# Performance work log

Measured on AMD Instinct MI355X. Metric: run time of the kernel, lower is better.

The kernel has to match this reference:

```python
import jax, jax.numpy as jnp
import numpy as np

H = 32      # num attention heads
HD = 64     # head dim
RD = 16     # rotary dim = 0.25 * head_dim (partial rotary)
EPS = 1e-5
BASE = 10000.0


def _ln(x, w, b):
    m = x.mean(-1, keepdims=True)
    v = ((x - m) ** 2).mean(-1, keepdims=True)
    return (x - m) / jnp.sqrt(v + EPS) * w + b


def _rot_half(x):
    x1, x2 = jnp.split(x, 2, axis=-1)
    return jnp.concatenate([-x2, x1], axis=-1)


def setup_inputs() -> dict:
    key = jax.random.key(0)
    ks = jax.random.split(key, 16)
    B, S, D, FF = 1, 2048, 2048, 8192
    std = 0.02
    hidden_states = jax.random.normal(ks[0], (B, S, D), jnp.float32)
    memory = jax.random.normal(ks[1], (B, S, D), jnp.float32)
    # causal additive mask (B,1,S,S): 0 where allowed, -inf above diagonal
    causal = jnp.where(jnp.tril(jnp.ones((S, S), bool)), 0.0, -jnp.inf).astype(jnp.float32)
    attention_mask = jnp.broadcast_to(causal[None, None], (B, 1, S, S))
    position_ids = jnp.broadcast_to(jnp.arange(S, dtype=jnp.int32), (B, S))
    return {
        'hidden_states': hidden_states,
        'memory': memory,
        'attention_mask': attention_mask,
        'position_ids': position_ids,
        'ln1_w': jnp.ones((D,), jnp.float32),
        'ln1_b': jnp.zeros((D,), jnp.float32),
        'ln2_w': jnp.ones((D,), jnp.float32),
        'ln2_b': jnp.zeros((D,), jnp.float32),
        'Wq': jax.random.normal(ks[2], (D, D), jnp.float32) * std,
        'Wk': jax.random.normal(ks[3], (D, D), jnp.float32) * std,
        'Wv': jax.random.normal(ks[4], (D, D), jnp.float32) * std,
        'Wo': jax.random.normal(ks[5], (D, D), jnp.float32) * std,
        'Wg': jax.random.normal(ks[6], (FF, D), jnp.float32) * std,
        'Wu': jax.random.normal(ks[7], (FF, D), jnp.float32) * std,
        'Wd': jax.random.normal(ks[8], (D, FF), jnp.float32) * std,
    }


def reference(hidden_states, memory, attention_mask, position_ids,
              ln1_w, ln1_b, ln2_w, ln2_b, Wq, Wk, Wv, Wo, Wg, Wu, Wd):
    B, S, D = hidden_states.shape
    residual = hidden_states
    h = _ln(hidden_states, ln1_w, ln1_b)
    mem = _ln(memory, ln1_w, ln1_b)

    # fast_forward: concat memory in front along sequence
    x = jnp.concatenate([mem, h], axis=1)              # (B, 2S, D)
    pos = jnp.concatenate([position_ids, position_ids], axis=1)  # (B, 2S)
    L = 2 * S

    q = (x @ Wq.T).reshape(B, L, H, HD).transpose(0, 2, 1, 3)  # (B,H,2S,HD)
    k = (x @ Wk.T).reshape(B, L, H, HD).transpose(0, 2, 1, 3)
    v = (x @ Wv.T).reshape(B, L, H, HD).transpose(0, 2, 1, 3)

    # partial rotary embedding
    inv_freq = 1.0 / (BASE ** (jnp.arange(0, RD, 2, dtype=jnp.float32) / RD))
    t = pos.astype(jnp.float32)[:, :, None] * inv_freq       # (B,2S,RD/2)
    emb = jnp.concatenate([t, t], axis=-1)                   # (B,2S,RD)
    cos = jnp.cos(emb)[:, None]                              # (B,1,2S,RD)
    sin = jnp.sin(emb)[:, None]
    qr, qp = q[..., :RD], q[..., RD:]
    kr, kp = k[..., :RD], k[..., RD:]
    qr = qr * cos + _rot_half(qr) * sin
    kr = kr * cos + _rot_half(kr) * sin
    q = jnp.concatenate([qr, qp], axis=-1)
    k = jnp.concatenate([kr, kp], axis=-1)

    # only non-memory queries attend
    q = q[:, :, S:]                                          # (B,H,S,HD)
    scores = jnp.einsum('bhqd,bhkd->bhqk', q, k) / jnp.sqrt(jnp.float32(HD))  # (B,H,S,2S)

    # left mask: causal + no attending to own memory slot; right: only own position (+ causal)
    eye = jnp.eye(S, dtype=bool)[None, None]
    left = jnp.where(eye, -jnp.inf, attention_mask)
    right = jnp.where(eye, attention_mask, -jnp.inf)
    mask = jnp.concatenate([left, right], axis=-1)           # (B,1,S,2S)

    w = jax.nn.softmax((scores + mask).astype(jnp.float32), axis=-1).astype(q.dtype)
    attn = jnp.einsum('bhqk,bhkd->bhqd', w, v)
    attn = attn.transpose(0, 2, 1, 3).reshape(B, S, D) @ Wo.T

    h = residual + attn
    residual2 = h
    h2 = _ln(h, ln2_w, ln2_b)
    mlp = (jax.nn.silu(h2 @ Wg.T) * (h2 @ Wu.T)) @ Wd.T
    return residual2 + mlp
```

## Files before the change

kernel.cpp:

```cpp
#include <hip/hip_runtime.h>
#include <stdint.h>
#include <stddef.h>

typedef short s16;
typedef __attribute__((ext_vector_type(8))) short short8;
typedef __attribute__((ext_vector_type(4))) float float4v;

#define S_LEN 2048
#define DMODEL 2048
#define LLEN 4096
#define FFDIM 8192
#define NHEAD 32
#define HDIM 64

#define AS1 __attribute__((address_space(1)))
#define AS3 __attribute__((address_space(3)))

__device__ __forceinline__ float bf2f(short s) {
  union { uint32_t u; float f; } x;
  x.u = ((uint32_t)(uint16_t)s) << 16;
  return x.f;
}
__device__ __forceinline__ short f2bf(float f) {
  union { float f; uint32_t u; } x;
  x.f = f;
  uint32_t r = x.u + 0x7fffu + ((x.u >> 16) & 1u);
  return (short)(r >> 16);
}

template <typename T> __device__ __forceinline__ float ldv(const T* p, size_t i);
template <> __device__ __forceinline__ float ldv<float>(const float* p, size_t i) { return p[i]; }
template <> __device__ __forceinline__ float ldv<s16>(const s16* p, size_t i) { return bf2f(p[i]); }
template <typename T> __device__ __forceinline__ void stv(T* p, size_t i, float v);
template <> __device__ __forceinline__ void stv<float>(float* p, size_t i, float v) { p[i] = v; }
template <> __device__ __forceinline__ void stv<s16>(s16* p, size_t i, float v) { p[i] = f2bf(v); }

__global__ __launch_bounds__(256) void w2bf(const float* __restrict__ src, s16* __restrict__ dst,
                                            int n8) {
  const int i = blockIdx.x * 256 + threadIdx.x;
  if (i >= n8) return;
  const float4v a = ((const float4v*)src)[2 * i];
  const float4v b = ((const float4v*)src)[2 * i + 1];
  short8 o;
#pragma unroll
  for (int j = 0; j < 4; j++) { o[j] = f2bf(a[j]); o[j + 4] = f2bf(b[j]); }
  ((short8*)dst)[i] = o;
}

template <typename T>
__global__ __launch_bounds__(256) void ln_kernel(const T* __restrict__ src,
                                                 const float* __restrict__ w,
                                                 const float* __restrict__ b,
                                                 s16* __restrict__ dst) {
  const int row = blockIdx.x, t = threadIdx.x;
  float v[8];
  float s = 0.f, s2 = 0.f;
#pragma unroll
  for (int i = 0; i < 8; i++) {
    v[i] = ldv<T>(src, (size_t)row * DMODEL + t * 8 + i);
    s += v[i];
    s2 += v[i] * v[i];
  }
#pragma unroll
  for (int off = 32; off > 0; off >>= 1) {
    s += __shfl_down(s, off);
    s2 += __shfl_down(s2, off);
  }
  __shared__ float rs[4], rs2[4];
  if ((t & 63) == 0) { rs[t >> 6] = s; rs2[t >> 6] = s2; }
  __syncthreads();
  const float fs = rs[0] + rs[1] + rs[2] + rs[3];
  const float fs2 = rs2[0] + rs2[1] + rs2[2] + rs2[3];
  const float mean = fs * (1.f / (float)DMODEL);
  const float var = fs2 * (1.f / (float)DMODEL) - mean * mean;
  const float rstd = rsqrtf(var + 1e-5f);
  const float4v w0 = *(const float4v*)(w + t * 8);
  const float4v w1 = *(const float4v*)(w + t * 8 + 4);
  const float4v b0 = *(const float4v*)(b + t * 8);
  const float4v b1 = *(const float4v*)(b + t * 8 + 4);
  short8 o;
#pragma unroll
  for (int i = 0; i < 4; i++) {
    o[i] = f2bf((v[i] - mean) * rstd * w0[i] + b0[i]);
    o[i + 4] = f2bf((v[i + 4] - mean) * rstd * w1[i] + b1[i]);
  }
  *(short8*)(dst + (size_t)row * DMODEL + t * 8) = o;
}

__global__ __launch_bounds__(256) void init_out(float4v* __restrict__ dst,
                                                const float4v* __restrict__ src, int n4) {
  const int i = blockIdx.x * 256 + threadIdx.x;
  if (i < n4) dst[i] = src ? src[i] : float4v{0.f, 0.f, 0.f, 0.f};
}

template <typename T>
__global__ __launch_bounds__(256) void rope_kernel(T* __restrict__ buf, const int* __restrict__ pos,
                                                   int nrows) {
  const int idx = blockIdx.x * 256 + threadIdx.x;
  if (idx >= nrows * NHEAD) return;
  const int row = idx >> 5, h = idx & 31;
  const int pid = pos[row < S_LEN ? row : row - S_LEN];
  T* ptr = buf + (size_t)row * DMODEL + h * HDIM;
  float a[8], c[8];
  if constexpr (sizeof(T) == 2) {
    const short8 r0 = *(const short8*)ptr;
    const short8 r1 = *(const short8*)(ptr + 8);
#pragma unroll
    for (int f = 0; f < 8; f++) { a[f] = bf2f(r0[f]); c[f] = bf2f(r1[f]); }
  } else {
    const float4v x0 = *(const float4v*)ptr;
    const float4v x1 = *(const float4v*)(ptr + 4);
    const float4v x2 = *(const float4v*)(ptr + 8);
    const float4v x3 = *(const float4v*)(ptr + 12);
#pragma unroll
    for (int f = 0; f < 4; f++) { a[f] = x0[f]; a[f + 4] = x1[f]; c[f] = x2[f]; c[f + 4] = x3[f]; }
  }
  const float inv_freq[8] = {1.0f, 0.31622776601683794f, 0.1f, 0.031622776601683794f,
                             0.01f, 0.0031622776601683794f, 0.001f, 0.00031622776601683794f};
  const float fp = (float)pid;
  float o0[8], o1[8];
#pragma unroll
  for (int f = 0; f < 8; f++) {
    float sv, cv;
    sincosf(fp * inv_freq[f], &sv, &cv);
    o0[f] = a[f] * cv - c[f] * sv;
    o1[f] = c[f] * cv + a[f] * sv;
  }
  if constexpr (sizeof(T) == 2) {
    short8 w0, w1;
#pragma unroll
    for (int f = 0; f < 8; f++) { w0[f] = f2bf(o0[f]); w1[f] = f2bf(o1[f]); }
    *(short8*)ptr = w0;
    *(short8*)(ptr + 8) = w1;
  } else {
    float4v y0, y1, y2, y3;
#pragma unroll
    for (int f = 0; f < 4; f++) { y0[f] = o0[f]; y1[f] = o0[f + 4]; y2[f] = o1[f]; y3[f] = o1[f + 4]; }
    *(float4v*)ptr = y0;
    *(float4v*)(ptr + 4) = y1;
    *(float4v*)(ptr + 8) = y2;
    *(float4v*)(ptr + 12) = y3;
  }
}

template <int EPI, int BSRC, typename AUXT, typename OUTT>
__global__ __launch_bounds__(256) void gemm_bt(const s16* __restrict__ A, const void* __restrict__ Wp,
                                               OUTT* __restrict__ C, const AUXT* __restrict__ aux,
                                               int M, int N, int K) {
  __shared__ alignas(16) s16 As[3][128 * 32];
  __shared__ alignas(16) s16 Bs[3][128 * 32];
  const int t = threadIdx.x;
  const int wave = t >> 6, lane = t & 63;
  const int quad = lane >> 4, l15 = lane & 15;
  const int n0 = blockIdx.x * 128, m0 = blockIdx.y * 128;
  const int wm = wave >> 1, wn = wave & 1;
  const int srow = lane >> 2, skk = (lane & 3) * 8;
  const int br4 = t >> 2, bc4 = (t & 3) * 8;
  const int kchunk = K / (int)gridDim.z;
  const int kbeg = kchunk * (int)blockIdx.z;

  float4v acc[4][4];
#pragma unroll
  for (int i = 0; i < 4; i++)
#pragma unroll
    for (int j = 0; j < 4; j++) acc[i][j] = float4v{0.f, 0.f, 0.f, 0.f};

  const s16* Wb = (const s16*)Wp;

  if constexpr (BSRC == 1) {
    const int nsteps = kchunk >> 5;
    auto stage = [&](int buf, int k0) {
#pragma unroll
      for (int cc = 0; cc < 2; cc++) {
        const int ci = wave * 2 + cc;
        const s16* ga = A + (size_t)(m0 + ci * 16 + srow) * K + (k0 + skk);
        __builtin_amdgcn_global_load_lds((const AS1 void*)ga, (AS3 void*)(&As[buf][ci * 512]), 16, 0, 0);
        const s16* gb = Wb + (size_t)(n0 + ci * 16 + srow) * K + (k0 + skk);
        __builtin_amdgcn_global_load_lds((const AS1 void*)gb, (AS3 void*)(&Bs[buf][ci * 512]), 16, 0, 0);
      }
    };
    stage(0, kbeg);
    if (nsteps > 1) {
      stage(1, kbeg + 32);
      asm volatile("s_waitcnt vmcnt(4)" ::: "memory");
    } else {
      asm volatile("s_waitcnt vmcnt(0)" ::: "memory");
    }
    __builtin_amdgcn_s_barrier();
    asm volatile("" ::: "memory");
    int cur = 0;
    for (int s = 0; s < nsteps; ++s) {
      short8 a[4], b[4];
#pragma unroll
      for (int mt = 0; mt < 4; mt++)
        a[mt] = *(const short8*)&As[cur][(wm * 64 + mt * 16 + l15) * 32 + quad * 8];
#pragma unroll
      for (int nt = 0; nt < 4; nt++)
        b[nt] = *(const short8*)&Bs[cur][(wn * 64 + nt * 16 + l15) * 32 + quad * 8];
      if (s + 2 < nsteps) {
        int nb = cur + 2; if (nb >= 3) nb -= 3;
        stage(nb, kbeg + (s + 2) * 32);
      }
#pragma unroll
      for (int mt = 0; mt < 4; mt++)
#pragma unroll
        for (int nt = 0; nt < 4; nt++)
          acc[mt][nt] = __builtin_amdgcn_mfma_f32_16x16x32_bf16(a[mt], b[nt], acc[mt][nt], 0, 0, 0);
      if (s + 1 < nsteps) {
        if (s + 2 < nsteps) asm volatile("s_waitcnt vmcnt(4)" ::: "memory");
        else asm volatile("s_waitcnt vmcnt(0)" ::: "memory");
        __builtin_amdgcn_s_barrier();
        asm volatile("" ::: "memory");
      }
      cur = (cur == 2) ? 0 : cur + 1;
    }
  } else {
    const float* wrow0 = (const float*)Wp + (size_t)(n0 + br4) * K + bc4;
    const float* wrow1 = wrow0 + (size_t)64 * K;
    for (int k0 = kbeg; k0 < kbeg + kchunk; k0 += 32) {
      float4v wa0 = *(const float4v*)(wrow0 + k0);
      float4v wa1 = *(const float4v*)(wrow0 + k0 + 4);
      float4v wb0 = *(const float4v*)(wrow1 + k0);
      float4v wb1 = *(const float4v*)(wrow1 + k0 + 4);
      __syncthreads();
#pragma unroll
      for (int cc = 0; cc < 2; cc++) {
        const int ci = wave * 2 + cc;
        const s16* ga = A + (size_t)(m0 + ci * 16 + srow) * K + (k0 + skk);
        __builtin_amdgcn_global_load_lds((const AS1 void*)ga, (AS3 void*)(&As[0][ci * 512]), 16, 0, 0);
      }
      short8 c0, c1;
#pragma unroll
      for (int i = 0; i < 4; i++) {
        c0[i] = f2bf(wa0[i]);
        c0[i + 4] = f2bf(wa1[i]);
        c1[i] = f2bf(wb0[i]);
        c1[i + 4] = f2bf(wb1[i]);
      }
      *(short8*)&Bs[0][br4 * 32 + bc4] = c0;
      *(short8*)&Bs[0][(64 + br4) * 32 + bc4] = c1;
      __syncthreads();
      short8 a[4], b[4];
#pragma unroll
      for (int mt = 0; mt < 4; mt++)
        a[mt] = *(const short8*)&As[0][(wm * 64 + mt * 16 + l15) * 32 + quad * 8];
#pragma unroll
      for (int nt = 0; nt < 4; nt++)
        b[nt] = *(const short8*)&Bs[0][(wn * 64 + nt * 16 + l15) * 32 + quad * 8];
#pragma unroll
      for (int mt = 0; mt < 4; mt++)
#pragma unroll
        for (int nt = 0; nt < 4; nt++)
          acc[mt][nt] = __builtin_amdgcn_mfma_f32_16x16x32_bf16(a[mt], b[nt], acc[mt][nt], 0, 0, 0);
    }
  }
#pragma unroll
  for (int mt = 0; mt < 4; mt++) {
#pragma unroll
    for (int nt = 0; nt < 4; nt++) {
      const float* av = (const float*)&acc[mt][nt];
      const int col = n0 + wn * 64 + nt * 16 + l15;
      const int rowb = m0 + wm * 64 + mt * 16 + quad * 4;
#pragma unroll
      for (int r = 0; r < 4; r++) {
        const size_t idx = (size_t)(rowb + r) * N + col;
        float v = av[r];
        if constexpr (EPI == 3) {
          unsafeAtomicAdd((float*)&C[idx], v);
        } else {
          if (EPI == 1) v += ldv<AUXT>(aux, idx);
          if (EPI == 2) { const float g = ldv<AUXT>(aux, idx); v *= g / (1.0f + __expf(-g)); }
          stv<OUTT>(C, idx, v);
        }
      }
    }
  }
}

__global__ __launch_bounds__(256) void attn_kernel(const float* __restrict__ qb, const s16* __restrict__ kb,
                                                   const s16* __restrict__ vb, s16* __restrict__ attn) {
  __shared__ alignas(16) s16 Qs[64 * 72];
  __shared__ alignas(16) s16 Ks[64 * 72];
  __shared__ alignas(16) s16 Vt[64 * 72];
  __shared__ alignas(16) s16 Ps[64 * 72];
  const int t = threadIdx.x;
  const int h = blockIdx.x & 31;
  const int qblk = 31 - (int)(blockIdx.x >> 5);
  const int wave = t >> 6, lane = t & 63;
  const int quad = lane >> 4, l15 = lane & 15;

#pragma unroll
  for (int rr = 0; rr < 2; rr++) {
    const int tt = t + rr * 256;
    const int i = tt >> 3, d0 = (tt & 7) * 8;
    const float* qp = qb + (size_t)(qblk * 64 + i) * DMODEL + h * HDIM + d0;
    const float4v q0 = *(const float4v*)qp;
    const float4v q1 = *(const float4v*)(qp + 4);
    short8 o;
#pragma unroll
    for (int x = 0; x < 4; x++) { o[x] = f2bf(q0[x]); o[x + 4] = f2bf(q1[x]); }
    *(short8*)&Qs[i * 72 + d0] = o;
  }

  float4v O[4];
#pragma unroll
  for (int i = 0; i < 4; i++) O[i] = float4v{0.f, 0.f, 0.f, 0.f};
  float m_run[4] = {-1e30f, -1e30f, -1e30f, -1e30f};
  float l_run[4] = {0.f, 0.f, 0.f, 0.f};

  const float SCALE = 0.125f * 1.442695040888963f;

  const int j0 = t >> 3, d00 = (t & 7) * 8;
  const int vkeyw = (d00 >> 3) & 7;
  const size_t colb = (size_t)h * HDIM + d00;

  const int nchunks = qblk + 2;
  short8 kr0 = *(const short8*)(kb + (size_t)j0 * DMODEL + colb);
  short8 kr1 = *(const short8*)(kb + (size_t)(j0 + 32) * DMODEL + colb);
  short8 vr0 = *(const short8*)(vb + (size_t)j0 * DMODEL + colb);
  short8 vr1 = *(const short8*)(vb + (size_t)(j0 + 32) * DMODEL + colb);

  for (int c = 0; c < nchunks; ++c) {
    asm volatile("s_waitcnt lgkmcnt(0)" ::: "memory");
    __builtin_amdgcn_s_barrier();
    asm volatile("" ::: "memory");
    *(short8*)&Ks[j0 * 72 + d00] = kr0;
    *(short8*)&Ks[(j0 + 32) * 72 + d00] = kr1;
#pragma unroll
    for (int x = 0; x < 8; x++) {
      Vt[(d00 + x) * 72 + (j0 ^ (vkeyw << 3))] = vr0[x];
      Vt[(d00 + x) * 72 + ((j0 + 32) ^ (vkeyw << 3))] = vr1[x];
    }
    if (c + 1 < nchunks) {
      const int krow = (c + 1 <= qblk) ? (c + 1) * 64 : (S_LEN + qblk * 64);
      kr0 = *(const short8*)(kb + (size_t)(krow + j0) * DMODEL + colb);
      kr1 = *(const short8*)(kb + (size_t)(krow + j0 + 32) * DMODEL + colb);
      vr0 = *(const short8*)(vb + (size_t)(krow + j0) * DMODEL + colb);
      vr1 = *(const short8*)(vb + (size_t)(krow + j0 + 32) * DMODEL + colb);
    }
    asm volatile("s_waitcnt lgkmcnt(0)" ::: "memory");
    __builtin_amdgcn_s_barrier();
    asm volatile("" ::: "memory");

    float4v Sacc[4];
#pragma unroll
    for (int i = 0; i < 4; i++) Sacc[i] = float4v{0.f, 0.f, 0.f, 0.f};
    __builtin_amdgcn_s_setprio(1);
#pragma unroll
    for (int ks = 0; ks < 2; ks++) {
      const short8 af = *(const short8*)&Qs[(wave * 16 + l15) * 72 + ks * 32 + quad * 8];
#pragma unroll
      for (int nt = 0; nt < 4; nt++) {
        const short8 bf = *(const short8*)&Ks[(nt * 16 + l15) * 72 + ks * 32 + quad * 8];
        Sacc[nt] = __builtin_amdgcn_mfma_f32_16x16x32_bf16(af, bf, Sacc[nt], 0, 0, 0);
      }
    }
    __builtin_amdgcn_s_setprio(0);
    float* sp = (float*)Sacc;
    if (c < qblk) {
#pragma unroll
      for (int i = 0; i < 16; i++) sp[i] = fminf(sp[i] * SCALE, 2e4f);
    } else {
#pragma unroll
      for (int nt = 0; nt < 4; nt++)
#pragma unroll
        for (int r = 0; r < 4; r++) {
          const int il = wave * 16 + quad * 4 + r;
          const int jl = nt * 16 + l15;
          const bool ok = (c == qblk) ? (jl < il) : (jl == il);
          sp[nt * 4 + r] = ok ? fminf(sp[nt * 4 + r] * SCALE, 2e4f) : -1e30f;
        }
    }
#pragma unroll
    for (int r = 0; r < 4; r++) {
      float mx = fmaxf(fmaxf(sp[0 * 4 + r], sp[1 * 4 + r]), fmaxf(sp[2 * 4 + r], sp[3 * 4 + r]));
#pragma unroll
      for (int off = 1; off < 16; off <<= 1) mx = fmaxf(mx, __shfl_xor(mx, off));
      const float mnew = fmaxf(m_run[r], mx);
      float alpha, sum;
      if (mnew < -1e29f) {
        alpha = 1.f; sum = 0.f;
#pragma unroll
        for (int nt = 0; nt < 4; nt++) sp[nt * 4 + r] = 0.f;
      } else {
        alpha = exp2f(m_run[r] - mnew);
        m_run[r] = mnew;
        sum = 0.f;
#pragma unroll
        for (int nt = 0; nt < 4; nt++) {
          const float p = exp2f(sp[nt * 4 + r] - mnew);
          sp[nt * 4 + r] = p;
          sum += p;
        }
      }
#pragma unroll
      for (int off = 1; off < 16; off <<= 1) sum += __shfl_xor(sum, off);
      l_run[r] = l_run[r] * alpha + sum;
      float* op = (float*)O;
#pragma unroll
      for (int dt = 0; dt < 4; dt++) op[dt * 4 + r] *= alpha;
    }
#pragma unroll
    for (int nt = 0; nt < 4; nt++)
#pragma unroll
      for (int r = 0; r < 4; r++)
        Ps[(wave * 16 + quad * 4 + r) * 72 + nt * 16 + l15] = f2bf(sp[nt * 4 + r]);
    __builtin_amdgcn_s_setprio(1);
#pragma unroll
    for (int ks = 0; ks < 2; ks++) {
      const short8 pf = *(const short8*)&Ps[(wave * 16 + l15) * 72 + ks * 32 + quad * 8];
#pragma unroll
      for (int dt = 0; dt < 4; dt++) {
        const int dd = dt * 16 + l15;
        const int vkey = (dd >> 3) & 7;
        const short8 vf = *(const short8*)&Vt[dd * 72 + ((ks * 32 + quad * 8) ^ (vkey << 3))];
        O[dt] = __builtin_amdgcn_mfma_f32_16x16x32_bf16(pf, vf, O[dt], 0, 0, 0);
      }
    }
    __builtin_amdgcn_s_setprio(0);
  }
  const float* op = (const float*)O;
#pragma unroll
  for (int dt = 0; dt < 4; dt++)
#pragma unroll
    for (int r = 0; r < 4; r++) {
      const int row = qblk * 64 + wave * 16 + quad * 4 + r;
      const int col = h * HDIM + dt * 16 + l15;
      const float inv_l = 1.0f / fmaxf(l_run[r], 1e-20f);
      attn[(size_t)row * DMODEL + col] = f2bf(op[dt * 4 + r] * inv_l);
    }
}

extern "C" void kernel_launch(void* const* d_in, const int* in_sizes, int n_in,
                              void* d_out, int out_size, void* d_ws, size_t ws_size,
                              hipStream_t stream) {
  const float* hidden = (const float*)d_in[0];
  const float* memory = (const float*)d_in[1];
  const int* pos_ids = (const int*)d_in[3];
  const float* ln1_w = (const float*)d_in[4];
  const float* ln1_b = (const float*)d_in[5];
  const float* ln2_w = (const float*)d_in[6];
  const float* ln2_b = (const float*)d_in[7];
  const float* Wq = (const float*)d_in[8];
  const float* Wk = (const float*)d_in[9];
  const float* Wv = (const float*)d_in[10];
  const float* Wo = (const float*)d_in[11];
  const float* Wg = (const float*)d_in[12];
  const float* Wu = (const float*)d_in[13];
  const float* Wd = (const float*)d_in[14];
  s16* ws = (s16*)d_ws;
  const size_t M1 = (size_t)1024 * 1024;

  s16* x = ws;
  float* q = (float*)d_out;
  s16* k = ws + 8 * M1;
  s16* v = ws + 16 * M1;
  s16* attn = ws;
  s16* h2 = ws + 4 * M1;
  s16* g = ws + 8 * M1;

  const bool bw = ws_size >= (size_t)88 * M1 * sizeof(s16);
  s16* Wqb = ws + 24 * M1;
  s16* Wkb = Wqb + 4 * M1;
  s16* Wvb = Wkb + 4 * M1;
  s16* Wob = Wvb + 4 * M1;
  s16* Wgb = Wob + 4 * M1;
  s16* Wub = Wgb + 16 * M1;
  s16* Wdb = Wub + 16 * M1;

  if (bw) {
    w2bf<<<2048, 256, 0, stream>>>(Wq, Wqb, 512 * 1024);
    w2bf<<<2048, 256, 0, stream>>>(Wk, Wkb, 512 * 1024);
    w2bf<<<2048, 256, 0, stream>>>(Wv, Wvb, 512 * 1024);
    w2bf<<<2048, 256, 0, stream>>>(Wo, Wob, 512 * 1024);
    w2bf<<<8192, 256, 0, stream>>>(Wg, Wgb, 2048 * 1024);
    w2bf<<<8192, 256, 0, stream>>>(Wu, Wub, 2048 * 1024);
    w2bf<<<8192, 256, 0, stream>>>(Wd, Wdb, 2048 * 1024);
  }

  ln_kernel<float><<<S_LEN, 256, 0, stream>>>(memory, ln1_w, ln1_b, x);
  ln_kernel<float><<<S_LEN, 256, 0, stream>>>(hidden, ln1_w, ln1_b, x + (size_t)S_LEN * DMODEL);
  init_out<<<4096, 256, 0, stream>>>((float4v*)d_out, (const float4v*)nullptr, 1 << 20);
  if (bw) {
    gemm_bt<3, 1, float, float><<<dim3(16, 16, 4), 256, 0, stream>>>(x + (size_t)S_LEN * DMODEL, Wqb, q, (const float*)nullptr, S_LEN, DMODEL, DMODEL);
    gemm_bt<0, 1, s16, s16><<<dim3(16, 32), 256, 0, stream>>>(x, Wkb, k, (const s16*)nullptr, LLEN, DMODEL, DMODEL);
    gemm_bt<0, 1, s16, s16><<<dim3(16, 32), 256, 0, stream>>>(x, Wvb, v, (const s16*)nullptr, LLEN, DMODEL, DMODEL);
  } else {
    gemm_bt<3, 0, float, float><<<dim3(16, 16, 4), 256, 0, stream>>>(x + (size_t)S_LEN * DMODEL, Wq, q, (const float*)nullptr, S_LEN, DMODEL, DMODEL);
    gemm_bt<0, 0, s16, s16><<<dim3(16, 32), 256, 0, stream>>>(x, Wk, k, (const s16*)nullptr, LLEN, DMODEL, DMODEL);
    gemm_bt<0, 0, s16, s16><<<dim3(16, 32), 256, 0, stream>>>(x, Wv, v, (const s16*)nullptr, LLEN, DMODEL, DMODEL);
  }
  rope_kernel<float><<<(S_LEN * NHEAD) / 256, 256, 0, stream>>>(q, pos_ids, S_LEN);
  rope_kernel<s16><<<(LLEN * NHEAD) / 256, 256, 0, stream>>>(k, pos_ids, LLEN);
  attn_kernel<<<NHEAD * (S_LEN / 64), 256, 0, stream>>>(q, k, v, attn);
  init_out<<<4096, 256, 0, stream>>>((float4v*)d_out, (const float4v*)hidden, 1 << 20);
  if (bw)
    gemm_bt<3, 1, float, float><<<dim3(16, 16, 4), 256, 0, stream>>>(attn, Wob, (float*)d_out, (const float*)nullptr, S_LEN, DMODEL, DMODEL);
  else
    gemm_bt<3, 0, float, float><<<dim3(16, 16, 4), 256, 0, stream>>>(attn, Wo, (float*)d_out, (const float*)nullptr, S_LEN, DMODEL, DMODEL);
  ln_kernel<float><<<S_LEN, 256, 0, stream>>>((const float*)d_out, ln2_w, ln2_b, h2);
  if (bw) {
    gemm_bt<0, 1, s16, s16><<<dim3(64, 16), 256, 0, stream>>>(h2, Wgb, g, (const s16*)nullptr, S_LEN, FFDIM, DMODEL);
    gemm_bt<2, 1, s16, s16><<<dim3(64, 16), 256, 0, stream>>>(h2, Wub, g, g, S_LEN, FFDIM, DMODEL);
    gemm_bt<3, 1, float, float><<<dim3(16, 16, 4), 256, 0, stream>>>(g, Wdb, (float*)d_out, (const float*)nullptr, S_LEN, DMODEL, FFDIM);
  } else {
    gemm_bt<0, 0, s16, s16><<<dim3(64, 16), 256, 0, stream>>>(h2, Wg, g, (const s16*)nullptr, S_LEN, FFDIM, DMODEL);
    gemm_bt<2, 0, s16, s16><<<dim3(64, 16), 256, 0, stream>>>(h2, Wu, g, g, S_LEN, FFDIM, DMODEL);
    gemm_bt<3, 0, float, float><<<dim3(16, 16, 4), 256, 0, stream>>>(g, Wd, (float*)d_out, (const float*)nullptr, S_LEN, DMODEL, FFDIM);
  }
}
```

Before: 942.5 us.

## Use 256x256 tiled 512-thread GEMM with 4-stage pipeline and fused K/V projection

Adds a bf16-weight GEMM kernel with 256x256 output tiles, 8 waves and a 4-deep LDS prefetch ring, and uses it for all projection GEMMs on the bf16-weight path. K and V projections become one GEMM over contiguous Wk|Wv bf16 weights, writing an interleaved KV buffer with a 2*D leading dimension. Rope and attention now take that stride. The larger tiles raise operand reuse per load but use more LDS and registers and give fewer blocks per GEMM.

```diff
diff --git a/kernel.cpp b/kernel.cpp
--- a/kernel.cpp
+++ b/kernel.cpp
@@ -95,12 +95,12 @@
 
 template <typename T>
 __global__ __launch_bounds__(256) void rope_kernel(T* __restrict__ buf, const int* __restrict__ pos,
-                                                   int nrows) {
+                                                   int nrows, int ld) {
   const int idx = blockIdx.x * 256 + threadIdx.x;
   if (idx >= nrows * NHEAD) return;
   const int row = idx >> 5, h = idx & 31;
   const int pid = pos[row < S_LEN ? row : row - S_LEN];
-  T* ptr = buf + (size_t)row * DMODEL + h * HDIM;
+  T* ptr = buf + (size_t)row * ld + h * HDIM;
   float a[8], c[8];
   if constexpr (sizeof(T) == 2) {
     const short8 r0 = *(const short8*)ptr;
@@ -143,124 +143,78 @@
   }
 }
 
-template <int EPI, int BSRC, typename AUXT, typename OUTT>
-__global__ __launch_bounds__(256) void gemm_bt(const s16* __restrict__ A, const void* __restrict__ Wp,
-                                               OUTT* __restrict__ C, const AUXT* __restrict__ aux,
-                                               int M, int N, int K) {
-  __shared__ alignas(16) s16 As[3][128 * 32];
-  __shared__ alignas(16) s16 Bs[3][128 * 32];
+template <int EPI, typename AUXT, typename OUTT>
+__global__ __launch_bounds__(512, 2) void gemm_bt2(const s16* __restrict__ A, const s16* __restrict__ W,
+                                                   OUTT* __restrict__ C, const AUXT* __restrict__ aux,
+                                                   int M, int N, int K) {
+  __shared__ alignas(16) s16 As[4][256 * 32];
+  __shared__ alignas(16) s16 Bs[4][256 * 32];
   const int t = threadIdx.x;
   const int wave = t >> 6, lane = t & 63;
   const int quad = lane >> 4, l15 = lane & 15;
-  const int n0 = blockIdx.x * 128, m0 = blockIdx.y * 128;
-  const int wm = wave >> 1, wn = wave & 1;
+  const int n0 = blockIdx.x * 256, m0 = blockIdx.y * 256;
+  const int wm = wave >> 2, wn = wave & 3;
   const int srow = lane >> 2, skk = (lane & 3) * 8;
-  const int br4 = t >> 2, bc4 = (t & 3) * 8;
   const int kchunk = K / (int)gridDim.z;
   const int kbeg = kchunk * (int)blockIdx.z;
-
-  float4v acc[4][4];
-#pragma unroll
-  for (int i = 0; i < 4; i++)
+  const int nsteps = kchunk >> 5;
+
+  float4v acc[8][4];
+#pragma unroll
+  for (int i = 0; i < 8; i++)
 #pragma unroll
     for (int j = 0; j < 4; j++) acc[i][j] = float4v{0.f, 0.f, 0.f, 0.f};
 
-  const s16* Wb = (const s16*)Wp;
-
-  if constexpr (BSRC == 1) {
-    const int nsteps = kchunk >> 5;
-    auto stage = [&](int buf, int k0) {
-#pragma unroll
-      for (int cc = 0; cc < 2; cc++) {
-        const int ci = wave * 2 + cc;
-        const s16* ga = A + (size_t)(m0 + ci * 16 + srow) * K + (k0 + skk);
-        __builtin_amdgcn_global_load_lds((const AS1 void*)ga, (AS3 void*)(&As[buf][ci * 512]), 16, 0, 0);
-        const s16* gb = Wb + (size_t)(n0 + ci * 16 + srow) * K + (k0 + skk);
-        __builtin_amdgcn_global_load_lds((const AS1 void*)gb, (AS3 void*)(&Bs[buf][ci * 512]), 16, 0, 0);
-      }
-    };
-    stage(0, kbeg);
-    if (nsteps > 1) {
-      stage(1, kbeg + 32);
-      asm volatile("s_waitcnt vmcnt(4)" ::: "memory");
-    } else {
-      asm volatile("s_waitcnt vmcnt(0)" ::: "memory");
-    }
-    __builtin_amdgcn_s_barrier();
-    asm volatile("" ::: "memory");
-    int cur = 0;
-    for (int s = 0; s < nsteps; ++s) {
-      short8 a[4], b[4];
-#pragma unroll
-      for (int mt = 0; mt < 4; mt++)
-        a[mt] = *(const short8*)&As[cur][(wm * 64 + mt * 16 + l15) * 32 + quad * 8];
+  auto stage = [&](int buf, int k0) {
+#pragma unroll
+    for (int cc = 0; cc < 2; cc++) {
+      const int ci = wave * 2 + cc;
+      const s16* ga = A + (size_t)(m0 + ci * 16 + srow) * K + (k0 + skk);
+      __builtin_amdgcn_global_load_lds((const AS1 void*)ga, (AS3 void*)(&As[buf][ci * 512]), 16, 0, 0);
+      const s16* gb = W + (size_t)(n0 + ci * 16 + srow) * K + (k0 + skk);
+      __builtin_amdgcn_global_load_lds((const AS1 void*)gb, (AS3 void*)(&Bs[buf][ci * 512]), 16, 0, 0);
+    }
+  };
+  stage(0, kbeg);
+  if (nsteps > 1) stage(1, kbeg + 32);
+  if (nsteps > 2) stage(2, kbeg + 64);
+  if (nsteps > 2) asm volatile("s_waitcnt vmcnt(8)" ::: "memory");
+  else if (nsteps > 1) asm volatile("s_waitcnt vmcnt(4)" ::: "memory");
+  else asm volatile("s_waitcnt vmcnt(0)" ::: "memory");
+  __builtin_amdgcn_s_barrier();
+  asm volatile("" ::: "memory");
+
+  int cur = 0;
+  for (int s = 0; s < nsteps; ++s) {
+    short8 a[8], b[4];
+#pragma unroll
+    for (int mt = 0; mt < 8; mt++)
+      a[mt] = *(const short8*)&As[cur][(wm * 128 + mt * 16 + l15) * 32 + quad * 8];
+#pragma unroll
+    for (int nt = 0; nt < 4; nt++)
+      b[nt] = *(const short8*)&Bs[cur][(wn * 64 + nt * 16 + l15) * 32 + quad * 8];
+    if (s + 3 < nsteps) stage((cur + 3) & 3, kbeg + (s + 3) * 32);
+#pragma unroll
+    for (int mt = 0; mt < 8; mt++)
 #pragma unroll
       for (int nt = 0; nt < 4; nt++)
-        b[nt] = *(const short8*)&Bs[cur][(wn * 64 + nt * 16 + l15) * 32 + quad * 8];
-      if (s + 2 < nsteps) {
-        int nb = cur + 2; if (nb >= 3) nb -= 3;
-        stage(nb, kbeg + (s + 2) * 32);
-      }
-#pragma unroll
-      for (int mt = 0; mt < 4; mt++)
-#pragma unroll
-        for (int nt = 0; nt < 4; nt++)
-          acc[mt][nt] = __builtin_amdgcn_mfma_f32_16x16x32_bf16(a[mt], b[nt], acc[mt][nt], 0, 0, 0);
-      if (s + 1 < nsteps) {
-        if (s + 2 < nsteps) asm volatile("s_waitcnt vmcnt(4)" ::: "memory");
-        else asm volatile("s_waitcnt vmcnt(0)" ::: "memory");
-        __builtin_amdgcn_s_barrier();
-        asm volatile("" ::: "memory");
-      }
-      cur = (cur == 2) ? 0 : cur + 1;
-    }
-  } else {
-    const float* wrow0 = (const float*)Wp + (size_t)(n0 + br4) * K + bc4;
-    const float* wrow1 = wrow0 + (size_t)64 * K;
-    for (int k0 = kbeg; k0 < kbeg + kchunk; k0 += 32) {
-      float4v wa0 = *(const float4v*)(wrow0 + k0);
-      float4v wa1 = *(const float4v*)(wrow0 + k0 + 4);
-      float4v wb0 = *(const float4v*)(wrow1 + k0);
-      float4v wb1 = *(const float4v*)(wrow1 + k0 + 4);
-      __syncthreads();
-#pragma unroll
-      for (int cc = 0; cc < 2; cc++) {
-        const int ci = wave * 2 + cc;
-        const s16* ga = A + (size_t)(m0 + ci * 16 + srow) * K + (k0 + skk);
-        __builtin_amdgcn_global_load_lds((const AS1 void*)ga, (AS3 void*)(&As[0][ci * 512]), 16, 0, 0);
-      }
-      short8 c0, c1;
-#pragma unroll
-      for (int i = 0; i < 4; i++) {
-        c0[i] = f2bf(wa0[i]);
-        c0[i + 4] = f2bf(wa1[i]);
-        c1[i] = f2bf(wb0[i]);
-        c1[i + 4] = f2bf(wb1[i]);
-      }
-      *(short8*)&Bs[0][br4 * 32 + bc4] = c0;
-      *(short8*)&Bs[0][(64 + br4) * 32 + bc4] = c1;
-      __syncthreads();
-      short8 a[4], b[4];
-#pragma unroll
-      for (int mt = 0; mt < 4; mt++)
-        a[mt] = *(const short8*)&As[0][(wm * 64 + mt * 16 + l15) * 32 + quad * 8];
-#pragma unroll
-      for (int nt = 0; nt < 4; nt++)
-        b[nt] = *(const short8*)&Bs[0][(wn * 64 + nt * 16 + l15) * 32 + quad * 8];
-#pragma unroll
-      for (int mt = 0; mt < 4; mt++)
-#pragma unroll
-        for (int nt = 0; nt < 4; nt++)
-          acc[mt][nt] = __builtin_amdgcn_mfma_f32_16x16x32_bf16(a[mt], b[nt], acc[mt][nt], 0, 0, 0);
-    }
-  }
-#pragma unroll
-  for (int mt = 0; mt < 4; mt++) {
+        acc[mt][nt] = __builtin_amdgcn_mfma_f32_16x16x32_bf16(a[mt], b[nt], acc[mt][nt], 0, 0, 0);
+    if (s + 1 < nsteps) {
+      if (s + 3 < nsteps) asm volatile("s_waitcnt vmcnt(8)" ::: "memory");
+      else if (s + 2 < nsteps) asm volatile("s_waitcnt vmcnt(4)" ::: "memory");
+      else asm volatile("s_waitcnt vmcnt(0)" ::: "memory");
+      __builtin_amdgcn_s_barrier();
+      asm volatile("" ::: "memory");
+    }
+    cur = (cur + 1) & 3;
+  }
+#pragma unroll
+  for (int mt = 0; mt < 8; mt++) {
 #pragma unroll
     for (int nt = 0; nt < 4; nt++) {
       const float* av = (const float*)&acc[mt][nt];
       const int col = n0 + wn * 64 + nt * 16 + l15;
-      const int rowb = m0 + wm * 64 + mt * 16 + quad * 4;
+      const int rowb = m0 + wm * 128 + mt * 16 + quad * 4;
 #pragma unroll
       for (int r = 0; r < 4; r++) {
         const size_t idx = (size_t)(rowb + r) * N + col;
@@ -277,8 +231,92 @@
   }
 }
 
+template <int EPI, typename AUXT, typename OUTT>
+__global__ __launch_bounds__(256) void gemm_bt(const s16* __restrict__ A, const float* __restrict__ W,
+                                               OUTT* __restrict__ C, const AUXT* __restrict__ aux,
+                                               int M, int N, int K) {
+  __shared__ alignas(16) s16 As[128 * 32];
+  __shared__ alignas(16) s16 Bs[128 * 32];
+  const int t = threadIdx.x;
+  const int wave = t >> 6, lane = t & 63;
+  const int quad = lane >> 4, l15 = lane & 15;
+  const int n0 = blockIdx.x * 128, m0 = blockIdx.y * 128;
+  const int wm = wave >> 1, wn = wave & 1;
+  const int srow = lane >> 2, skk = (lane & 3) * 8;
+  const int br4 = t >> 2, bc4 = (t & 3) * 8;
+  const int kchunk = K / (int)gridDim.z;
+  const int kbeg = kchunk * (int)blockIdx.z;
+
+  float4v acc[4][4];
+#pragma unroll
+  for (int i = 0; i < 4; i++)
+#pragma unroll
+    for (int j = 0; j < 4; j++) acc[i][j] = float4v{0.f, 0.f, 0.f, 0.f};
+
+  const float* wrow0 = W + (size_t)(n0 + br4) * K + bc4;
+  const float* wrow1 = wrow0 + (size_t)64 * K;
+  for (int k0 = kbeg; k0 < kbeg + kchunk; k0 += 32) {
+    float4v wa0 = *(const float4v*)(wrow0 + k0);
+    float4v wa1 = *(const float4v*)(wrow0 + k0 + 4);
+    float4v wb0 = *(const float4v*)(wrow1 + k0);
+    float4v wb1 = *(const float4v*)(wrow1 + k0 + 4);
+    __syncthreads();
+#pragma unroll
+    for (int cc = 0; cc < 2; cc++) {
+      const int ci = wave * 2 + cc;
+      const s16* ga = A + (size_t)(m0 + ci * 16 + srow) * K + (k0 + skk);
+      __builtin_amdgcn_global_load_lds((const AS1 void*)ga, (AS3 void*)(&As[ci * 512]), 16, 0, 0);
+    }
+    short8 c0, c1;
+#pragma unroll
+    for (int i = 0; i < 4; i++) {
+      c0[i] = f2bf(wa0[i]);
+      c0[i + 4] = f2bf(wa1[i]);
+      c1[i] = f2bf(wb0[i]);
+      c1[i + 4] = f2bf(wb1[i]);
+    }
+    *(short8*)&Bs[br4 * 32 + bc4] = c0;
+    *(short8*)&Bs[(64 + br4) * 32 + bc4] = c1;
+    __syncthreads();
+    short8 a[4], b[4];
+#pragma unroll
+    for (int mt = 0; mt < 4; mt++)
+      a[mt] = *(const short8*)&As[(wm * 64 + mt * 16 + l15) * 32 + quad * 8];
+#pragma unroll
+    for (int nt = 0; nt < 4; nt++)
+      b[nt] = *(const short8*)&Bs[(wn * 64 + nt * 16 + l15) * 32 + quad * 8];
+#pragma unroll
+    for (int mt = 0; mt < 4; mt++)
+#pragma unroll
+      for (int nt = 0; nt < 4; nt++)
+        acc[mt][nt] = __builtin_amdgcn_mfma_f32_16x16x32_bf16(a[mt], b[nt], acc[mt][nt], 0, 0, 0);
+  }
+#pragma unroll
+  for (int mt = 0; mt < 4; mt++) {
+#pragma unroll
+    for (int nt = 0; nt < 4; nt++) {
+      const float* av = (const float*)&acc[mt][nt];
+      const int col = n0 + wn * 64 + nt * 16 + l15;
+      const int rowb = m0 + wm * 64 + mt * 16 + quad * 4;
+#pragma unroll
+      for (int r = 0; r < 4; r++) {
+        const size_t idx = (size_t)(rowb + r) * N + col;
+        float v = av[r];
+        if constexpr (EPI == 3) {
+          unsafeAtomicAdd((float*)&C[idx], v);
+        } else {
+          if (EPI == 1) v += ldv<AUXT>(aux, idx);
+          if (EPI == 2) { const float g = ldv<AUXT>(aux, idx); v *= g / (1.0f + __expf(-g)); }
+          stv<OUTT>(C, idx, v);
+        }
+      }
+    }
+  }
+}
+
 __global__ __launch_bounds__(256) void attn_kernel(const float* __restrict__ qb, const s16* __restrict__ kb,
-                                                   const s16* __restrict__ vb, s16* __restrict__ attn) {
+                                                   const s16* __restrict__ vb, s16* __restrict__ attn,
+                                                   int ldk) {
   __shared__ alignas(16) s16 Qs[64 * 72];
   __shared__ alignas(16) s16 Ks[64 * 72];
   __shared__ alignas(16) s16 Vt[64 * 72];
@@ -315,10 +353,10 @@
   const size_t colb = (size_t)h * HDIM + d00;
 
   const int nchunks = qblk + 2;
-  short8 kr0 = *(const short8*)(kb + (size_t)j0 * DMODEL + colb);
-  short8 kr1 = *(const short8*)(kb + (size_t)(j0 + 32) * DMODEL + colb);
-  short8 vr0 = *(const short8*)(vb + (size_t)j0 * DMODEL + colb);
-  short8 vr1 = *(const short8*)(vb + (size_t)(j0 + 32) * DMODEL + colb);
+  short8 kr0 = *(const short8*)(kb + (size_t)j0 * ldk + colb);
+  short8 kr1 = *(const short8*)(kb + (size_t)(j0 + 32) * ldk + colb);
+  short8 vr0 = *(const short8*)(vb + (size_t)j0 * ldk + colb);
+  short8 vr1 = *(const short8*)(vb + (size_t)(j0 + 32) * ldk + colb);
 
   for (int c = 0; c < nchunks; ++c) {
     asm volatile("s_waitcnt lgkmcnt(0)" ::: "memory");
@@ -333,10 +371,10 @@
     }
     if (c + 1 < nchunks) {
       const int krow = (c + 1 <= qblk) ? (c + 1) * 64 : (S_LEN + qblk * 64);
-      kr0 = *(const short8*)(kb + (size_t)(krow + j0) * DMODEL + colb);
-      kr1 = *(const short8*)(kb + (size_t)(krow + j0 + 32) * DMODEL + colb);
-      vr0 = *(const short8*)(vb + (size_t)(krow + j0) * DMODEL + colb);
-      vr1 = *(const short8*)(vb + (size_t)(krow + j0 + 32) * DMODEL + colb);
+      kr0 = *(const short8*)(kb + (size_t)(krow + j0) * ldk + colb);
+      kr1 = *(const short8*)(kb + (size_t)(krow + j0 + 32) * ldk + colb);
+      vr0 = *(const short8*)(vb + (size_t)(krow + j0) * ldk + colb);
+      vr1 = *(const short8*)(vb + (size_t)(krow + j0 + 32) * ldk + colb);
     }
     asm volatile("s_waitcnt lgkmcnt(0)" ::: "memory");
     __builtin_amdgcn_s_barrier();
@@ -453,8 +491,7 @@
 
   s16* x = ws;
   float* q = (float*)d_out;
-  s16* k = ws + 8 * M1;
-  s16* v = ws + 16 * M1;
+  s16* kv = ws + 8 * M1;
   s16* attn = ws;
   s16* h2 = ws + 4 * M1;
   s16* g = ws + 8 * M1;
@@ -482,30 +519,32 @@
   ln_kernel<float><<<S_LEN, 256, 0, stream>>>(hidden, ln1_w, ln1_b, x + (size_t)S_LEN * DMODEL);
   init_out<<<4096, 256, 0, stream>>>((float4v*)d_out, (const float4v*)nullptr, 1 << 20);
   if (bw) {
-    gemm_bt<3, 1, float, float><<<dim3(16, 16, 4), 256, 0, stream>>>(x + (size_t)S_LEN * DMODEL, Wqb, q, (const float*)nullptr, S_LEN, DMODEL, DMODEL);
-    gemm_bt<0, 1, s16, s16><<<dim3(16, 32), 256, 0, stream>>>(x, Wkb, k, (const s16*)nullptr, LLEN, DMODEL, DMODEL);
-    gemm_bt<0, 1, s16, s16><<<dim3(16, 32), 256, 0, stream>>>(x, Wvb, v, (const s16*)nullptr, LLEN, DMODEL, DMODEL);
+    gemm_bt2<3, float, float><<<dim3(8, 8, 4), 512, 0, stream>>>(x + (size_t)S_LEN * DMODEL, Wqb, q, (const float*)nullptr, S_LEN, DMODEL, DMODEL);
+    gemm_bt2<0, s16, s16><<<dim3(16, 16), 512, 0, stream>>>(x, Wkb, kv, (const s16*)nullptr, LLEN, 2 * DMODEL, DMODEL);
   } else {
-    gemm_bt<3, 0, float, float><<<dim3(16, 16, 4), 256, 0, stream>>>(x + (size_t)S_LEN * DMODEL, Wq, q, (const float*)nullptr, S_LEN, DMODEL, DMODEL);
-    gemm_bt<0, 0, s16, s16><<<dim3(16, 32), 256, 0, stream>>>(x, Wk, k, (const s16*)nullptr, LLEN, DMODEL, DMODEL);
-    gemm_bt<0, 0, s16, s16><<<dim3(16, 32), 256, 0, stream>>>(x, Wv, v, (const s16*)nullptr, LLEN, DMODEL, DMODEL);
-  }
-  rope_kernel<float><<<(S_LEN * NHEAD) / 256, 256, 0, stream>>>(q, pos_ids, S_LEN);
-  rope_kernel<s16><<<(LLEN * NHEAD) / 256, 256, 0, stream>>>(k, pos_ids, LLEN);
-  attn_kernel<<<NHEAD * (S_LEN / 64), 256, 0, stream>>>(q, k, v, attn);
+    gemm_bt<3, float, float><<<dim3(16, 16, 4), 256, 0, stream>>>(x + (size_t)S_LEN * DMODEL, Wq, q, (const float*)nullptr, S_LEN, DMODEL, DMODEL);
+    gemm_bt<0, s16, s16><<<dim3(16, 32), 256, 0, stream>>>(x, Wk, kv, (const s16*)nullptr, LLEN, DMODEL, DMODEL);
+    gemm_bt<0, s16, s16><<<dim3(16, 32), 256, 0, stream>>>(x, Wv, kv + 8 * M1, (const s16*)nullptr, LLEN, DMODEL, DMODEL);
+  }
+  const int ldk = bw ? 2 * DMODEL : DMODEL;
+  s16* kb = kv;
+  s16* vb = bw ? (kv + DMODEL) : (kv + 8 * M1);
+  rope_kernel<float><<<(S_LEN * NHEAD) / 256, 256, 0, stream>>>(q, pos_ids, S_LEN, DMODEL);
+  rope_kernel<s16><<<(LLEN * NHEAD) / 256, 256, 0, stream>>>(kb, pos_ids, LLEN, ldk);
+  attn_kernel<<<NHEAD * (S_LEN / 64), 256, 0, stream>>>(q, kb, vb, attn, ldk);
   init_out<<<4096, 256, 0, stream>>>((float4v*)d_out, (const float4v*)hidden, 1 << 20);
   if (bw)
-    gemm_bt<3, 1, float, float><<<dim3(16, 16, 4), 256, 0, stream>>>(attn, Wob, (float*)d_out, (const float*)nullptr, S_LEN, DMODEL, DMODEL);
+    gemm_bt2<3, float, float><<<dim3(8, 8, 4), 512, 0, stream>>>(attn, Wob, (float*)d_out, (const float*)nullptr, S_LEN, DMODEL, DMODEL);
   else
-    gemm_bt<3, 0, float, float><<<dim3(16, 16, 4), 256, 0, stream>>>(attn, Wo, (float*)d_out, (const float*)nullptr, S_LEN, DMODEL, DMODEL);
+    gemm_bt<3, float, float><<<dim3(16, 16, 4), 256, 0, stream>>>(attn, Wo, (float*)d_out, (const float*)nullptr, S_LEN, DMODEL, DMODEL);
   ln_kernel<float><<<S_LEN, 256, 0, stream>>>((const float*)d_out, ln2_w, ln2_b, h2);
   if (bw) {
-    gemm_bt<0, 1, s16, s16><<<dim3(64, 16), 256, 0, stream>>>(h2, Wgb, g, (const s16*)nullptr, S_LEN, FFDIM, DMODEL);
-    gemm_bt<2, 1, s16, s16><<<dim3(64, 16), 256, 0, stream>>>(h2, Wub, g, g, S_LEN, FFDIM, DMODEL);
-    gemm_bt<3, 1, float, float><<<dim3(16, 16, 4), 256, 0, stream>>>(g, Wdb, (float*)d_out, (const float*)nullptr, S_LEN, DMODEL, FFDIM);
+    gemm_bt2<0, s16, s16><<<dim3(32, 8), 512, 0, stream>>>(h2, Wgb, g, (const s16*)nullptr, S_LEN, FFDIM, DMODEL);
+    gemm_bt2<2, s16, s16><<<dim3(32, 8), 512, 0, stream>>>(h2, Wub, g, g, S_LEN, FFDIM, DMODEL);
+    gemm_bt2<3, float, float><<<dim3(8, 8, 4), 512, 0, stream>>>(g, Wdb, (float*)d_out, (const float*)nullptr, S_LEN, DMODEL, FFDIM);
   } else {
-    gemm_bt<0, 0, s16, s16><<<dim3(64, 16), 256, 0, stream>>>(h2, Wg, g, (const s16*)nullptr, S_LEN, FFDIM, DMODEL);
-    gemm_bt<2, 0, s16, s16><<<dim3(64, 16), 256, 0, stream>>>(h2, Wu, g, g, S_LEN, FFDIM, DMODEL);
-    gemm_bt<3, 0, float, float><<<dim3(16, 16, 4), 256, 0, stream>>>(g, Wd, (float*)d_out, (const float*)nullptr, S_LEN, DMODEL, FFDIM);
-  }
-}
+    gemm_bt<0, s16, s16><<<dim3(64, 16), 256, 0, stream>>>(h2, Wg, g, (const s16*)nullptr, S_LEN, FFDIM, DMODEL);
+    gemm_bt<2, s16, s16><<<dim3(64, 16), 256, 0, stream>>>(h2, Wu, g, g, S_LEN, FFDIM, DMODEL);
+    gemm_bt<3, float, float><<<dim3(16, 16, 4), 256, 0, stream>>>(g, Wd, (float*)d_out, (const float*)nullptr, S_LEN, DMODEL, FFDIM);
+  }
+}
```

After: 902.7 us. -4.2%, faster.
